# Optimization experiments

Hardware: AMD Instinct MI355X
Metric: run time of the kernel (lower is better)

The kernel has to match this reference:

```python
import jax, jax.numpy as jnp
import numpy as np

B, N, M = 64, 900, 300
NUM_CLASSES = 91  # labels_pred has num_classes+1 = 92 channels
POS_W, IOU_W, CLS_W = 1.0, 1.0, 1.0


def setup_inputs() -> dict:
    key = jax.random.key(0)
    k1, k2, k3, k4 = jax.random.split(key, 4)
    bbox_pred = jax.random.uniform(k1, (B, N, 4), dtype=jnp.float32)          # cxcywh
    labels_pred = jax.nn.softmax(jax.random.normal(k2, (B, N, NUM_CLASSES + 1), dtype=jnp.float32), axis=-1)
    bbox_gt = jax.random.uniform(k3, (B, M, 4), dtype=jnp.float32)
    labels_gt = jax.random.randint(k4, (B, M), 0, NUM_CLASSES + 1, dtype=jnp.int32)
    return {"bbox_pred": bbox_pred, "labels_pred": labels_pred,
            "bbox_gt": bbox_gt, "labels_gt": labels_gt}


def _corners(b):
    # b: [..., 4] in cxcywh -> upper-left, down-right corners
    ul = b[..., 0:2] - 0.5 * b[..., 2:4]
    dr = b[..., 0:2] + 0.5 * b[..., 2:4]
    return ul, dr


def reference(bbox_pred, labels_pred, bbox_gt, labels_gt):
    # --- pairwise L1 bbox cost: [B, N, M] ---
    bbox_loss = jnp.sum(jnp.abs(bbox_pred[:, :, None, :] - bbox_gt[:, None, :, :]), axis=-1)

    # --- pairwise (negative) GIoU-style cost, with the original '+1' pixel convention ---
    p_ul, p_dr = _corners(bbox_pred)   # [B, N, 2]
    g_ul, g_dr = _corners(bbox_gt)     # [B, M, 2]
    pu, pd = p_ul[:, :, None, :], p_dr[:, :, None, :]   # [B, N, 1, 2]
    gu, gd = g_ul[:, None, :, :], g_dr[:, None, :, :]   # [B, 1, M, 2]

    inter_wh = jnp.maximum(jnp.minimum(pd, gd) - jnp.maximum(pu, gu) + 1.0, 0.0)
    inter_area = inter_wh[..., 0] * inter_wh[..., 1]                 # [B, N, M]

    p_wh = jnp.maximum(p_dr - p_ul + 1.0, 0.0)
    p_area = p_wh[..., 0] * p_wh[..., 1]                             # [B, N]
    g_wh = jnp.maximum(g_dr - g_ul + 1.0, 0.0)
    g_area = g_wh[..., 0] * g_wh[..., 1]                             # [B, M]

    union = p_area[:, :, None] + g_area[:, None, :] - inter_area     # [B, N, M]
    iou = inter_area / union

    bound_wh = jnp.maximum(jnp.maximum(pd, gd) - jnp.minimum(pu, gu) + 1.0, 0.0)
    bound_area = bound_wh[..., 0] * bound_wh[..., 1]                 # [B, N, M]
    bg_ratio = (bound_area - union) / bound_area
    iou_loss = -(iou - bg_ratio)                                     # [B, N, M]

    # --- class cost: -labels_pred[b, n, labels_gt[b, m]]  (gather, no while_loop) ---
    class_loss = -jax.vmap(lambda lp, lg: lp[:, lg])(labels_pred, labels_gt)  # [B, N, M]

    cost = POS_W * bbox_loss + IOU_W * iou_loss + CLS_W * class_loss
    return cost
```

## Files before the change

### kernel.cpp

```cpp
#include <hip/hip_runtime.h>

#define BB   64
#define NN   900
#define MM   300
#define NC1  92
#define MQ   (MM / 4)
#define KN   4
#define NCH  (NN / KN)

__global__ __launch_bounds__(256) void cost_kernel(
    const float4* __restrict__ bbox_pred,
    const float*  __restrict__ labels_pred,
    const float4* __restrict__ bbox_gt,
    const int4*   __restrict__ labels_gt,
    float4*       __restrict__ out)
{
    const int total = BB * NCH * MQ;
    int idx = blockIdx.x * blockDim.x + threadIdx.x;
    if (idx >= total) return;

    int mq   = idx % MQ;
    int rest = idx / MQ;
    int b    = rest / NCH;
    int nb   = rest % NCH;

    int4 lg = labels_gt[b * MQ + mq];
    int lbl[4] = { lg.x, lg.y, lg.z, lg.w };

    float gx[4], gy[4], gz[4], gw_[4];
    float gux[4], guy[4], gdx[4], gdy[4], ga[4];
#pragma unroll
    for (int j = 0; j < 4; ++j) {
        float4 g = bbox_gt[b * MM + mq * 4 + j];
        gx[j] = g.x; gy[j] = g.y; gz[j] = g.z; gw_[j] = g.w;
        gux[j] = g.x - 0.5f * g.z;  guy[j] = g.y - 0.5f * g.w;
        gdx[j] = g.x + 0.5f * g.z;  gdy[j] = g.y + 0.5f * g.w;
        float gwd = fmaxf(gdx[j] - gux[j] + 1.0f, 0.0f);
        float ghd = fmaxf(gdy[j] - guy[j] + 1.0f, 0.0f);
        ga[j] = gwd * ghd;
    }

#pragma unroll
    for (int k = 0; k < KN; ++k) {
        int n  = nb * KN + k;
        int bn = b * NN + n;

        float4 p = bbox_pred[bn];
        float pux = p.x - 0.5f * p.z, puy = p.y - 0.5f * p.w;
        float pdx = p.x + 0.5f * p.z, pdy = p.y + 0.5f * p.w;
        float pw = fmaxf(pdx - pux + 1.0f, 0.0f);
        float ph = fmaxf(pdy - puy + 1.0f, 0.0f);
        float p_area = pw * ph;

        const float* lp_row = labels_pred + (size_t)bn * NC1;

        float res[4];
#pragma unroll
        for (int j = 0; j < 4; ++j) {
            float bbox_loss = fabsf(p.x - gx[j]) + fabsf(p.y - gy[j])
                            + fabsf(p.z - gz[j]) + fabsf(p.w - gw_[j]);

            float iwx = fmaxf(fminf(pdx, gdx[j]) - fmaxf(pux, gux[j]) + 1.0f, 0.0f);
            float iwy = fmaxf(fminf(pdy, gdy[j]) - fmaxf(puy, guy[j]) + 1.0f, 0.0f);
            float inter = iwx * iwy;

            float uni = p_area + ga[j] - inter;
            float iou = inter * __builtin_amdgcn_rcpf(uni);

            float bwx = fmaxf(fmaxf(pdx, gdx[j]) - fminf(pux, gux[j]) + 1.0f, 0.0f);
            float bwy = fmaxf(fmaxf(pdy, gdy[j]) - fminf(puy, guy[j]) + 1.0f, 0.0f);
            float barea = bwx * bwy;
            float bg = (barea - uni) * __builtin_amdgcn_rcpf(barea);

            float cls = lp_row[lbl[j]];
            res[j] = bbox_loss + (bg - iou) - cls;
        }

        out[(size_t)bn * MQ + mq] = make_float4(res[0], res[1], res[2], res[3]);
    }
}

extern "C" void kernel_launch(void* const* d_in, const int* in_sizes, int n_in,
                              void* d_out, int out_size, void* d_ws, size_t ws_size,
                              hipStream_t stream) {
    const float4* bbox_pred   = (const float4*)d_in[0];
    const float*  labels_pred = (const float*) d_in[1];
    const float4* bbox_gt     = (const float4*)d_in[2];
    const int4*   labels_gt   = (const int4*)  d_in[3];
    float4*       out         = (float4*)d_out;

    const int total = BB * NCH * MQ;
    const int block = 256;
    const int grid  = (total + block - 1) / block;
    cost_kernel<<<grid, block, 0, stream>>>(bbox_pred, labels_pred, bbox_gt,
                                            labels_gt, out);
}
```

Baseline: 29.93 us.

## Simplify GIoU algebra, raise per-thread rows, and use nontemporal output stores

Rewrites the GIoU terms algebraically: the enclosing box width is obtained as the sum of both widths minus the raw intersection width, so the separate max/min bound computation goes away. The +1 offsets are folded into precomputed corners and areas, and the final expression becomes 1 - union/bound - iou. Each thread now handles 6 prediction rows instead of 4, and output stores use nontemporal hints to avoid cache pollution on the large write. The algebra drops the max(...,0) clamps on the area and bound widths, which assumes nonnegative box sizes, and the wider per-thread work lowers thread count and may raise register pressure.

```diff
diff --git a/kernel.cpp b/kernel.cpp
--- a/kernel.cpp
+++ b/kernel.cpp
@@ -5,15 +5,17 @@
 #define MM   300
 #define NC1  92
 #define MQ   (MM / 4)
-#define KN   4
+#define KN   6
 #define NCH  (NN / KN)
+
+typedef float floatx4 __attribute__((ext_vector_type(4)));
 
 __global__ __launch_bounds__(256) void cost_kernel(
     const float4* __restrict__ bbox_pred,
     const float*  __restrict__ labels_pred,
     const float4* __restrict__ bbox_gt,
     const int4*   __restrict__ labels_gt,
-    float4*       __restrict__ out)
+    floatx4*      __restrict__ out)
 {
     const int total = BB * NCH * MQ;
     int idx = blockIdx.x * blockDim.x + threadIdx.x;
@@ -28,55 +30,58 @@
     int lbl[4] = { lg.x, lg.y, lg.z, lg.w };
 
     float gx[4], gy[4], gz[4], gw_[4];
-    float gux[4], guy[4], gdx[4], gdy[4], ga[4];
+    float gux[4], guy[4], gdx1[4], gdy1[4];
+    float gz1[4], gw1[4], ga[4];
 #pragma unroll
     for (int j = 0; j < 4; ++j) {
         float4 g = bbox_gt[b * MM + mq * 4 + j];
         gx[j] = g.x; gy[j] = g.y; gz[j] = g.z; gw_[j] = g.w;
-        gux[j] = g.x - 0.5f * g.z;  guy[j] = g.y - 0.5f * g.w;
-        gdx[j] = g.x + 0.5f * g.z;  gdy[j] = g.y + 0.5f * g.w;
-        float gwd = fmaxf(gdx[j] - gux[j] + 1.0f, 0.0f);
-        float ghd = fmaxf(gdy[j] - guy[j] + 1.0f, 0.0f);
-        ga[j] = gwd * ghd;
+        gux[j]  = g.x - 0.5f * g.z;   guy[j]  = g.y - 0.5f * g.w;
+        gdx1[j] = g.x + 0.5f * g.z + 1.0f;
+        gdy1[j] = g.y + 0.5f * g.w + 1.0f;
+        gz1[j]  = g.z + 1.0f;         gw1[j]  = g.w + 1.0f;
+        ga[j]   = gz1[j] * gw1[j];
     }
 
 #pragma unroll
     for (int k = 0; k < KN; ++k) {
-        int n  = nb * KN + k;
-        int bn = b * NN + n;
+        int bn = b * NN + nb * KN + k;
 
         float4 p = bbox_pred[bn];
-        float pux = p.x - 0.5f * p.z, puy = p.y - 0.5f * p.w;
-        float pdx = p.x + 0.5f * p.z, pdy = p.y + 0.5f * p.w;
-        float pw = fmaxf(pdx - pux + 1.0f, 0.0f);
-        float ph = fmaxf(pdy - puy + 1.0f, 0.0f);
-        float p_area = pw * ph;
+        float pux  = p.x - 0.5f * p.z,  puy  = p.y - 0.5f * p.w;
+        float pdx1 = p.x + 0.5f * p.z + 1.0f;
+        float pdy1 = p.y + 0.5f * p.w + 1.0f;
+        float pz1  = p.z + 1.0f,        pw1  = p.w + 1.0f;
+        float p_area = pz1 * pw1;
 
         const float* lp_row = labels_pred + (size_t)bn * NC1;
 
         float res[4];
 #pragma unroll
         for (int j = 0; j < 4; ++j) {
-            float bbox_loss = fabsf(p.x - gx[j]) + fabsf(p.y - gy[j])
-                            + fabsf(p.z - gz[j]) + fabsf(p.w - gw_[j]);
-
-            float iwx = fmaxf(fminf(pdx, gdx[j]) - fmaxf(pux, gux[j]) + 1.0f, 0.0f);
-            float iwy = fmaxf(fminf(pdy, gdy[j]) - fmaxf(puy, guy[j]) + 1.0f, 0.0f);
+            float iwrx = fminf(pdx1, gdx1[j]) - fmaxf(pux, gux[j]);
+            float iwry = fminf(pdy1, gdy1[j]) - fmaxf(puy, guy[j]);
+            float iwx  = fmaxf(iwrx, 0.0f);
+            float iwy  = fmaxf(iwry, 0.0f);
             float inter = iwx * iwy;
 
-            float uni = p_area + ga[j] - inter;
+            float bwx = (pz1 + gz1[j]) - iwrx;
+            float bwy = (pw1 + gw1[j]) - iwry;
+            float barea = bwx * bwy;
+
+            float uni = (p_area + ga[j]) - inter;
             float iou = inter * __builtin_amdgcn_rcpf(uni);
+            float t   = uni   * __builtin_amdgcn_rcpf(barea);
 
-            float bwx = fmaxf(fmaxf(pdx, gdx[j]) - fminf(pux, gux[j]) + 1.0f, 0.0f);
-            float bwy = fmaxf(fmaxf(pdy, gdy[j]) - fminf(puy, guy[j]) + 1.0f, 0.0f);
-            float barea = bwx * bwy;
-            float bg = (barea - uni) * __builtin_amdgcn_rcpf(barea);
+            float bbox = fabsf(p.x - gx[j]) + fabsf(p.y - gy[j])
+                       + fabsf(p.z - gz[j]) + fabsf(p.w - gw_[j]);
 
             float cls = lp_row[lbl[j]];
-            res[j] = bbox_loss + (bg - iou) - cls;
+            res[j] = bbox + (1.0f - cls) - t - iou;
         }
 
-        out[(size_t)bn * MQ + mq] = make_float4(res[0], res[1], res[2], res[3]);
+        floatx4 v = { res[0], res[1], res[2], res[3] };
+        __builtin_nontemporal_store(v, &out[(size_t)bn * MQ + mq]);
     }
 }
 
@@ -87,7 +92,7 @@
     const float*  labels_pred = (const float*) d_in[1];
     const float4* bbox_gt     = (const float4*)d_in[2];
     const int4*   labels_gt   = (const int4*)  d_in[3];
-    float4*       out         = (float4*)d_out;
+    floatx4*      out         = (floatx4*)d_out;
 
     const int total = BB * NCH * MQ;
     const int block = 256;
```

After: 28.37 us. -5.2%, faster.
